# Optimization experiments

Measured on AMD Instinct MI355X. Metric: run time of the kernel, lower is better.

Reference implementation:

```python
import jax, jax.numpy as jnp
import numpy as np

NUM_EXPERTS = 8
D_MODEL = 1024
D_HIDDEN = 4096
TOP_K = 2
BATCH, SEQ = 2, 4096
T = BATCH * SEQ


def setup_inputs() -> dict:
    key = jax.random.key(0)
    k_x, k_p, k_i, k_wu, k_wd = jax.random.split(key, 5)
    x = jax.random.normal(k_x, (BATCH, SEQ, D_MODEL), dtype=jnp.float32)
    p = jax.random.uniform(k_p, (T, TOP_K), dtype=jnp.float32)
    expert_p = p / jnp.sum(p, axis=-1, keepdims=True)  # normalized gates over top-k
    expert_idxs = jax.random.randint(k_i, (T, TOP_K), 0, NUM_EXPERTS, dtype=jnp.int64)
    # ParallelExperts weight banks (stored as [E, in, out] for x @ W convention)
    w_up = jax.random.normal(k_wu, (NUM_EXPERTS, D_MODEL, D_HIDDEN), dtype=jnp.float32) * (D_MODEL ** -0.5)
    w_down = jax.random.normal(k_wd, (NUM_EXPERTS, D_HIDDEN, D_MODEL), dtype=jnp.float32) * (D_HIDDEN ** -0.5)
    return {"x": x, "expert_p": expert_p, "expert_idxs": expert_idxs,
            "w_up": w_up, "w_down": w_down}


def reference(x, expert_p, expert_idxs, w_up, w_down):
    """MoE MLP: for each token t and each of its top-k experts e=idx[t,k]:
       y[t] += p[t,k] * (gelu(x[t] @ Wup[e]) @ Wdown[e]).
       Expressed as a loop over the small fixed expert set with per-expert
       gate masses (mathematically identical to sort+grouped-GEMM dispatch)."""
    x_shape = x.shape
    xf = x.reshape(-1, x_shape[-1])  # [T, d]
    num_experts = w_up.shape[0]
    y = jnp.zeros_like(xf)
    for e in range(num_experts):
        # total gate mass routed from each token to expert e (0 if not routed)
        gate_e = jnp.sum(expert_p * (expert_idxs == e), axis=-1)  # [T]
        h = jax.nn.gelu(xf @ w_up[e], approximate=False)          # [T, hidden]
        y = y + gate_e[:, None] * (h @ w_down[e])                 # [T, d]
    return y.reshape(x_shape)
```

## Files before the change

kernel.cpp:

```cpp
#include <hip/hip_runtime.h>
#include <hip/hip_bf16.h>
#include <stdint.h>

#define NE 8
#define DM 1024
#define DH 4096
#define T_TOK 8192
#define NA 16384
#define BM 128
#define BN 128
#define BK 64
#define MT 20

typedef __attribute__((ext_vector_type(8))) short short8;
typedef __attribute__((ext_vector_type(4))) float f32x4;

typedef const __attribute__((address_space(1))) void cas1void;
typedef __attribute__((address_space(3))) void as3void;
#define GL2L(gp, lp) __builtin_amdgcn_global_load_lds((cas1void*)(uintptr_t)(gp), (as3void*)(uintptr_t)(lp), 16, 0, 0)

__device__ __forceinline__ unsigned short f2bf(float f) {
  union { float f; unsigned u; } v; v.f = f;
  unsigned r = (v.u + 0x7FFFu + ((v.u >> 16) & 1u)) >> 16;
  return (unsigned short)r;
}
__device__ __forceinline__ float geluf(float x) {
  float u = 0.7978845608028654f * x * (1.0f + 0.044715f * x * x);
  return x / (1.0f + __expf(-2.0f * u));
}

__global__ void k_route(const int* __restrict__ idx, const float* __restrict__ p,
                        int* __restrict__ offs, int* __restrict__ btok,
                        float* __restrict__ gate) {
  __shared__ int cnt[NE], cur[NE], off_s[NE];
  int tid = threadIdx.x;
  if (tid < NE) { cnt[tid] = 0; cur[tid] = 0; }
  __syncthreads();
  int e_loc[NA / 1024];
#pragma unroll
  for (int i = 0; i < NA / 1024; ++i) {
    int a = i * 1024 + tid;
    e_loc[i] = idx[a];
    atomicAdd(&cnt[e_loc[i]], 1);
  }
  __syncthreads();
  if (tid == 0) {
    int s = 0;
    for (int e = 0; e < NE; ++e) { off_s[e] = s; offs[e] = s; s += cnt[e]; }
    offs[NE] = s;
  }
  __syncthreads();
#pragma unroll
  for (int i = 0; i < NA / 1024; ++i) {
    int a = i * 1024 + tid;
    int e = e_loc[i];
    int pos = off_s[e] + atomicAdd(&cur[e], 1);
    btok[pos] = a >> 1;
    gate[pos] = p[a];
  }
}

__global__ void k_cvt_x(const float* __restrict__ x, unsigned short* __restrict__ xb) {
  int i = (blockIdx.x * 256 + threadIdx.x) * 8;
  float4 v0 = *(const float4*)(x + i);
  float4 v1 = *(const float4*)(x + i + 4);
  ushort4 o0, o1;
  o0.x = f2bf(v0.x); o0.y = f2bf(v0.y); o0.z = f2bf(v0.z); o0.w = f2bf(v0.w);
  o1.x = f2bf(v1.x); o1.y = f2bf(v1.y); o1.z = f2bf(v1.z); o1.w = f2bf(v1.w);
  *(ushort4*)(xb + i) = o0;
  *(ushort4*)(xb + i + 4) = o1;
}

__global__ void k_transpose2(const float* __restrict__ wup, const float* __restrict__ wdn,
                             unsigned short* __restrict__ wupT, unsigned short* __restrict__ wdnT) {
  __shared__ float tile[64][65];
  int z = blockIdx.z;
  const float* src; unsigned short* dst; int C, R, c0, r0;
  if (z < NE) {
    src = wup + (size_t)z * DM * DH; dst = wupT + (size_t)z * DM * DH;
    R = DM; C = DH; c0 = blockIdx.x * 64; r0 = blockIdx.y * 64;
  } else {
    src = wdn + (size_t)(z - NE) * DM * DH; dst = wdnT + (size_t)(z - NE) * DM * DH;
    R = DH; C = DM; c0 = (blockIdx.x & 15) * 64; r0 = (blockIdx.y * 4 + (blockIdx.x >> 4)) * 64;
  }
  int tid = threadIdx.x;
  int tr = tid >> 4;
  int tc = (tid & 15) * 4;
#pragma unroll
  for (int rr = 0; rr < 64; rr += 16) {
    float4 v = *(const float4*)(src + (size_t)(r0 + tr + rr) * C + c0 + tc);
    tile[tr + rr][tc + 0] = v.x; tile[tr + rr][tc + 1] = v.y;
    tile[tr + rr][tc + 2] = v.z; tile[tr + rr][tc + 3] = v.w;
  }
  __syncthreads();
#pragma unroll
  for (int cc = 0; cc < 64; cc += 16) {
    int oc = tr + cc;
    ushort4 o;
    o.x = f2bf(tile[tc + 0][oc]); o.y = f2bf(tile[tc + 1][oc]);
    o.z = f2bf(tile[tc + 2][oc]); o.w = f2bf(tile[tc + 3][oc]);
    *(ushort4*)(dst + (size_t)(c0 + oc) * R + r0 + tc) = o;
  }
}

template <int NKT>
__device__ __forceinline__ void gemm128(const unsigned short* const (&pA)[4],
                                        const unsigned short* const (&pB)[4],
                                        short* sA, short* sB, int w, int lane,
                                        f32x4 (&acc)[4][4]) {
  int wm = w & 1, wn = w >> 1;
  int lr = lane & 15, lg = lane >> 4;
  int wbase = w << 3;
  int arow = (wm * 64 + lr) * 64;
  int brow = (wn * 64 + lr) * 64;
  int swz = ((lr & 7) << 3);
#pragma unroll 1
  for (int kt = 0; kt < NKT; ++kt) {
#pragma unroll
    for (int r = 0; r < 4; ++r) {
      GL2L(pA[r] + kt * BK, sA + (r * 32 + wbase) * 64);
      GL2L(pB[r] + kt * BK, sB + (r * 32 + wbase) * 64);
    }
    __syncthreads();
#pragma unroll
    for (int kk = 0; kk < 2; ++kk) {
      int co = ((kk << 5) | (lg << 3)) ^ swz;
      short8 av[4], bv[4];
#pragma unroll
      for (int i = 0; i < 4; ++i) av[i] = *(const short8*)&sA[arow + i * 16 * 64 + co];
#pragma unroll
      for (int j = 0; j < 4; ++j) bv[j] = *(const short8*)&sB[brow + j * 16 * 64 + co];
#pragma unroll
      for (int i = 0; i < 4; ++i)
#pragma unroll
        for (int j = 0; j < 4; ++j)
          acc[i][j] = __builtin_amdgcn_mfma_f32_16x16x32_bf16(av[i], bv[j], acc[i][j], 0, 0, 0);
    }
    __syncthreads();
  }
}

__global__ __launch_bounds__(256, 3) void k_up(
    const unsigned short* __restrict__ xb, const unsigned short* __restrict__ wupT,
    const int* __restrict__ offs, const int* __restrict__ btok,
    unsigned short* __restrict__ h) {
  int e = blockIdx.x & 7;
  int r = blockIdx.x >> 3;
  int tile = r % MT, ny = r / MT;
  int beg = offs[e], cnt = offs[e + 1] - beg;
  int m0 = tile * BM;
  if (m0 >= cnt) return;
  int n0 = ny * BN;
  __align__(16) __shared__ short sA[BM * BK];
  __align__(16) __shared__ short sB[BN * BK];
  int tid = threadIdx.x;
  int w = tid >> 6, lane = tid & 63;
  int grp = tid >> 3, gran = tid & 7;
  int swcol = ((gran ^ (grp & 7)) << 3);
  const unsigned short* pA[4];
  const unsigned short* pB[4];
#pragma unroll
  for (int rr = 0; rr < 4; ++rr) {
    int row = rr * 32 + grp;
    int tok = btok[beg + min(m0 + row, cnt - 1)];
    pA[rr] = xb + (size_t)tok * DM + swcol;
    pB[rr] = wupT + ((size_t)e * DH + n0 + row) * DM + swcol;
  }
  f32x4 acc[4][4];
#pragma unroll
  for (int i = 0; i < 4; ++i)
#pragma unroll
    for (int j = 0; j < 4; ++j) acc[i][j] = (f32x4){0.f, 0.f, 0.f, 0.f};

  gemm128<DM / BK>(pA, pB, sA, sB, w, lane, acc);

  int wm = w & 1, wn = w >> 1;
  int lr = lane & 15, lg = lane >> 4;
#pragma unroll
  for (int i = 0; i < 4; ++i)
#pragma unroll
    for (int q = 0; q < 4; ++q) {
      int grow = wm * 64 + i * 16 + lg * 4 + q;
      if (m0 + grow < cnt) {
        size_t orow = (size_t)(beg + m0 + grow) * DH + n0;
#pragma unroll
        for (int j = 0; j < 4; ++j) {
          int col = wn * 64 + j * 16 + lr;
          h[orow + col] = f2bf(geluf(acc[i][j][q]));
        }
      }
    }
}

__global__ __launch_bounds__(256, 3) void k_down(
    const unsigned short* __restrict__ h, const unsigned short* __restrict__ wdnT,
    const int* __restrict__ offs, const int* __restrict__ btok,
    const float* __restrict__ gate, float* __restrict__ y) {
  int e = blockIdx.x & 7;
  int r = blockIdx.x >> 3;
  int tile = r % MT;
  int q2 = r / MT;
  int ny = q2 & 7, ks = q2 >> 3;
  int beg = offs[e], cnt = offs[e + 1] - beg;
  int m0 = tile * BM;
  if (m0 >= cnt) return;
  int n0 = ny * BN;
  int kbase = ks * (DH / 4);
  __align__(16) __shared__ short sA[BM * BK];
  __align__(16) __shared__ short sB[BN * BK];
  __shared__ int s_tok[BM];
  __shared__ float s_g[BM];
  int tid = threadIdx.x;
  if (tid < BM) {
    int rr = min(m0 + tid, cnt - 1);
    s_tok[tid] = btok[beg + rr];
    s_g[tid] = gate[beg + rr];
  }
  int w = tid >> 6, lane = tid & 63;
  int grp = tid >> 3, gran = tid & 7;
  int swcol = ((gran ^ (grp & 7)) << 3);
  const unsigned short* pA[4];
  const unsigned short* pB[4];
#pragma unroll
  for (int rr = 0; rr < 4; ++rr) {
    int row = rr * 32 + grp;
    int slot = beg + min(m0 + row, cnt - 1);
    pA[rr] = h + (size_t)slot * DH + kbase + swcol;
    pB[rr] = wdnT + ((size_t)e * DM + n0 + row) * DH + kbase + swcol;
  }
  f32x4 acc[4][4];
#pragma unroll
  for (int i = 0; i < 4; ++i)
#pragma unroll
    for (int j = 0; j < 4; ++j) acc[i][j] = (f32x4){0.f, 0.f, 0.f, 0.f};

  gemm128<(DH / 4) / BK>(pA, pB, sA, sB, w, lane, acc);

  int wm = w & 1, wn = w >> 1;
  int lr = lane & 15, lg = lane >> 4;
#pragma unroll
  for (int i = 0; i < 4; ++i)
#pragma unroll
    for (int q = 0; q < 4; ++q) {
      int grow = wm * 64 + i * 16 + lg * 4 + q;
      if (m0 + grow < cnt) {
        float g2 = s_g[grow];
        int tk = s_tok[grow];
#pragma unroll
        for (int j = 0; j < 4; ++j) {
          int col = n0 + wn * 64 + j * 16 + lr;
          atomicAdd(&y[(size_t)tk * DM + col], acc[i][j][q] * g2);
        }
      }
    }
}

extern "C" void kernel_launch(void* const* d_in, const int* in_sizes, int n_in,
                              void* d_out, int out_size, void* d_ws, size_t ws_size,
                              hipStream_t stream) {
  (void)in_sizes; (void)n_in; (void)ws_size;
  const float* x   = (const float*)d_in[0];
  const float* p   = (const float*)d_in[1];
  const int*   idx = (const int*)d_in[2];
  const float* wup = (const float*)d_in[3];
  const float* wdn = (const float*)d_in[4];
  float* y = (float*)d_out;
  char* ws = (char*)d_ws;
  int* offs   = (int*)(ws + 128);
  int* btok   = (int*)(ws + 256);
  float* gate = (float*)(ws + 256 + 65536);
  unsigned short* xb   = (unsigned short*)(ws + 131328);
  unsigned short* wupT = (unsigned short*)(ws + 131328 + 16777216);
  unsigned short* wdnT = wupT + (size_t)NE * DH * DM;
  unsigned short* h    = wdnT + (size_t)NE * DM * DH;

  hipMemsetAsync(d_out, 0, (size_t)out_size * sizeof(float), stream);
  k_route<<<1, 1024, 0, stream>>>(idx, p, offs, btok, gate);
  k_cvt_x<<<(T_TOK * DM) / (256 * 8), 256, 0, stream>>>(x, xb);
  k_transpose2<<<dim3(64, 16, 2 * NE), 256, 0, stream>>>(wup, wdn, wupT, wdnT);
  k_up<<<NE * MT * 32, 256, 0, stream>>>(xb, wupT, offs, btok, h);
  k_down<<<NE * MT * 32, 256, 0, stream>>>(h, wdnT, offs, btok, gate, y);
}
```

Before: 534.9 us.

## Replace atomic scatter in down-proj with bf16 partial buffer and merge kernel

```diff
diff --git a/kernel.cpp b/kernel.cpp
--- a/kernel.cpp
+++ b/kernel.cpp
@@ -24,14 +24,16 @@
   unsigned r = (v.u + 0x7FFFu + ((v.u >> 16) & 1u)) >> 16;
   return (unsigned short)r;
 }
+__device__ __forceinline__ float b2f(unsigned short u) {
+  union { unsigned u; float f; } v; v.u = (unsigned)u << 16; return v.f;
+}
 __device__ __forceinline__ float geluf(float x) {
   float u = 0.7978845608028654f * x * (1.0f + 0.044715f * x * x);
   return x / (1.0f + __expf(-2.0f * u));
 }
 
-__global__ void k_route(const int* __restrict__ idx, const float* __restrict__ p,
-                        int* __restrict__ offs, int* __restrict__ btok,
-                        float* __restrict__ gate) {
+__global__ void k_route(const int* __restrict__ idx, int* __restrict__ offs,
+                        int* __restrict__ btok, int* __restrict__ slotmap) {
   __shared__ int cnt[NE], cur[NE], off_s[NE];
   int tid = threadIdx.x;
   if (tid < NE) { cnt[tid] = 0; cur[tid] = 0; }
@@ -56,7 +58,7 @@
     int e = e_loc[i];
     int pos = off_s[e] + atomicAdd(&cur[e], 1);
     btok[pos] = a >> 1;
-    gate[pos] = p[a];
+    slotmap[a] = pos;
   }
 }
 
@@ -195,27 +197,20 @@
 __global__ __launch_bounds__(256, 3) void k_down(
     const unsigned short* __restrict__ h, const unsigned short* __restrict__ wdnT,
     const int* __restrict__ offs, const int* __restrict__ btok,
-    const float* __restrict__ gate, float* __restrict__ y) {
+    unsigned short* __restrict__ dws) {
   int e = blockIdx.x & 7;
   int r = blockIdx.x >> 3;
-  int tile = r % MT;
-  int q2 = r / MT;
+  int q2 = r & 15;
   int ny = q2 & 7, ks = q2 >> 3;
+  int tile = r >> 4;
   int beg = offs[e], cnt = offs[e + 1] - beg;
   int m0 = tile * BM;
   if (m0 >= cnt) return;
   int n0 = ny * BN;
-  int kbase = ks * (DH / 4);
+  int kbase = ks * (DH / 2);
   __align__(16) __shared__ short sA[BM * BK];
   __align__(16) __shared__ short sB[BN * BK];
-  __shared__ int s_tok[BM];
-  __shared__ float s_g[BM];
   int tid = threadIdx.x;
-  if (tid < BM) {
-    int rr = min(m0 + tid, cnt - 1);
-    s_tok[tid] = btok[beg + rr];
-    s_g[tid] = gate[beg + rr];
-  }
   int w = tid >> 6, lane = tid & 63;
   int grp = tid >> 3, gran = tid & 7;
   int swcol = ((gran ^ (grp & 7)) << 3);
@@ -234,31 +229,54 @@
 #pragma unroll
     for (int j = 0; j < 4; ++j) acc[i][j] = (f32x4){0.f, 0.f, 0.f, 0.f};
 
-  gemm128<(DH / 4) / BK>(pA, pB, sA, sB, w, lane, acc);
+  gemm128<(DH / 2) / BK>(pA, pB, sA, sB, w, lane, acc);
 
   int wm = w & 1, wn = w >> 1;
   int lr = lane & 15, lg = lane >> 4;
+  size_t kofs = (size_t)ks * NA * DM;
 #pragma unroll
   for (int i = 0; i < 4; ++i)
 #pragma unroll
     for (int q = 0; q < 4; ++q) {
       int grow = wm * 64 + i * 16 + lg * 4 + q;
       if (m0 + grow < cnt) {
-        float g2 = s_g[grow];
-        int tk = s_tok[grow];
+        size_t orow = kofs + (size_t)(beg + m0 + grow) * DM + n0;
 #pragma unroll
         for (int j = 0; j < 4; ++j) {
-          int col = n0 + wn * 64 + j * 16 + lr;
-          atomicAdd(&y[(size_t)tk * DM + col], acc[i][j][q] * g2);
+          int col = wn * 64 + j * 16 + lr;
+          dws[orow + col] = f2bf(acc[i][j][q]);
         }
       }
     }
 }
 
+__global__ __launch_bounds__(256) void k_merge(const unsigned short* __restrict__ dws,
+                                               const int* __restrict__ slotmap,
+                                               const float* __restrict__ p,
+                                               float* __restrict__ y) {
+  int t = blockIdx.x * 2 + (threadIdx.x >> 7);
+  int c0 = (threadIdx.x & 127) * 8;
+  int s0 = slotmap[2 * t], s1 = slotmap[2 * t + 1];
+  float g0 = p[2 * t], g1 = p[2 * t + 1];
+  const size_t KOFS = (size_t)NA * DM;
+  short8 a0 = *(const short8*)&dws[(size_t)s0 * DM + c0];
+  short8 a1 = *(const short8*)&dws[KOFS + (size_t)s0 * DM + c0];
+  short8 b0 = *(const short8*)&dws[(size_t)s1 * DM + c0];
+  short8 b1 = *(const short8*)&dws[KOFS + (size_t)s1 * DM + c0];
+  float out[8];
+#pragma unroll
+  for (int k = 0; k < 8; ++k)
+    out[k] = g0 * (b2f((unsigned short)a0[k]) + b2f((unsigned short)a1[k])) +
+             g1 * (b2f((unsigned short)b0[k]) + b2f((unsigned short)b1[k]));
+  float* yp = y + (size_t)t * DM + c0;
+  *(float4*)yp = make_float4(out[0], out[1], out[2], out[3]);
+  *(float4*)(yp + 4) = make_float4(out[4], out[5], out[6], out[7]);
+}
+
 extern "C" void kernel_launch(void* const* d_in, const int* in_sizes, int n_in,
                               void* d_out, int out_size, void* d_ws, size_t ws_size,
                               hipStream_t stream) {
-  (void)in_sizes; (void)n_in; (void)ws_size;
+  (void)in_sizes; (void)n_in; (void)ws_size; (void)out_size;
   const float* x   = (const float*)d_in[0];
   const float* p   = (const float*)d_in[1];
   const int*   idx = (const int*)d_in[2];
@@ -266,18 +284,19 @@
   const float* wdn = (const float*)d_in[4];
   float* y = (float*)d_out;
   char* ws = (char*)d_ws;
-  int* offs   = (int*)(ws + 128);
-  int* btok   = (int*)(ws + 256);
-  float* gate = (float*)(ws + 256 + 65536);
-  unsigned short* xb   = (unsigned short*)(ws + 131328);
-  unsigned short* wupT = (unsigned short*)(ws + 131328 + 16777216);
+  int* offs    = (int*)(ws + 128);
+  int* btok    = (int*)(ws + 256);
+  int* slotmap = (int*)(ws + 256 + 65536);
+  unsigned short* xb   = (unsigned short*)(ws + 256 + 131072);
+  unsigned short* wupT = xb + (size_t)T_TOK * DM;
   unsigned short* wdnT = wupT + (size_t)NE * DH * DM;
   unsigned short* h    = wdnT + (size_t)NE * DM * DH;
-
-  hipMemsetAsync(d_out, 0, (size_t)out_size * sizeof(float), stream);
-  k_route<<<1, 1024, 0, stream>>>(idx, p, offs, btok, gate);
+  unsigned short* dws  = wupT;
+
+  k_route<<<1, 1024, 0, stream>>>(idx, offs, btok, slotmap);
   k_cvt_x<<<(T_TOK * DM) / (256 * 8), 256, 0, stream>>>(x, xb);
   k_transpose2<<<dim3(64, 16, 2 * NE), 256, 0, stream>>>(wup, wdn, wupT, wdnT);
   k_up<<<NE * MT * 32, 256, 0, stream>>>(xb, wupT, offs, btok, h);
-  k_down<<<NE * MT * 32, 256, 0, stream>>>(h, wdnT, offs, btok, gate, y);
-}
+  k_down<<<NE * MT * 16, 256, 0, stream>>>(h, wdnT, offs, btok, dws);
+  k_merge<<<T_TOK / 2, 256, 0, stream>>>(dws, slotmap, p, y);
+}
```

New measurement: 438.4 us. -18.0%, faster.
